# Kernel tuning notes

Hardware: AMD Instinct MI355X
Metric: run time of the kernel (lower is better)

## Reference

```python
import jax, jax.numpy as jnp
import numpy as np

TAU = 0.25
VTH = 1.0

def setup_inputs() -> dict:
    key = jax.random.key(0)
    k1, k2 = jax.random.split(key)
    B, T, F, U = 256, 100, 1024, 1024
    x = jax.random.normal(k1, (B, T, F), dtype=jnp.float32)
    kernel = jax.random.normal(k2, (F, U), dtype=jnp.float32) * 0.02
    bias = jnp.zeros((U,), dtype=jnp.float32)
    return {"x": x, "kernel": kernel, "bias": bias}

def reference(x, kernel, bias):
    # x: [B, T, F]; one big GEMM for all timesteps, then sequential LIF scan.
    current = jnp.einsum('btf,fu->btu', x, kernel) + bias  # [B, T, U]
    B, T, U = current.shape
    v0 = jnp.zeros((B, U), dtype=x.dtype)

    def lif_step(voltage, cur_t):
        voltage = TAU * voltage + (1.0 - TAU) * cur_t
        spikes = (voltage > VTH).astype(cur_t.dtype)
        voltage = voltage - spikes * VTH
        return voltage, spikes

    _, spikes_t = jax.lax.scan(lif_step, v0, jnp.moveaxis(current, 1, 0))  # [T, B, U]
    output_spikes = jnp.moveaxis(spikes_t, 0, 1)  # [B, T, U]
    spike_counts = jnp.sum(output_spikes, axis=1)  # [B, U]
    return output_spikes, spike_counts
```

## Files before the change

### kernel.cpp

```cpp
#include <hip/hip_runtime.h>


#define UN 128
#define BK 16
#define CS 132
#define CHUNK 50
#define TMAX 100

__device__ __forceinline__ void gload_lds16(const float* g, float* l) {
    __builtin_amdgcn_global_load_lds(
        (const __attribute__((address_space(1))) void*)g,
        (__attribute__((address_space(3))) void*)l,
        16, 0, 0);
}

__global__ __launch_bounds__(256) void fused_snn(
    const float* __restrict__ x,
    const float* __restrict__ W,
    const float* __restrict__ bias,
    float* __restrict__ spikes,
    float* __restrict__ counts,
    int B, int T, int F, int U)
{
    __shared__ __align__(16) float smem[CHUNK * CS];
    float* As = smem;
    float* Ws = smem + 1600;

    const int tid = threadIdx.x;
    const int tg  = tid >> 4;
    const int ug  = tid & 15;
    const int u0  = blockIdx.x * UN;
    const int b   = blockIdx.y;

    float acc[7][8];
    #pragma unroll
    for (int i = 0; i < 7; i++)
        #pragma unroll
        for (int j = 0; j < 8; j++) acc[i][j] = 0.f;

    const float* xb = x + (size_t)b * T * F;

    const float* ga0 = xb + (size_t)(tid >> 2) * F + (tid & 3) * 4;
    const float* ga1 = xb + (size_t)(64 + (tid >> 2)) * F + (tid & 3) * 4;
    const float* gw0 = W + (size_t)(tid >> 5) * U + u0 + (tid & 31) * 4;
    const float* gw1 = W + (size_t)(8 + (tid >> 5)) * U + u0 + (tid & 31) * 4;
    float* la0 = As + tid * 4;
    float* la1 = As + (256 + tid) * 4;
    float* lw0 = Ws + tid * 4;
    float* lw1 = Ws + (256 + tid) * 4;
    const bool a1on = (tid < 144);
    const bool w0   = (tid < 64);

    for (int k0 = 0; k0 < F; k0 += BK) {
        gload_lds16(ga0 + k0, la0);
        if (a1on) gload_lds16(ga1 + k0, la1);
        gload_lds16(gw0 + (size_t)k0 * U, lw0);
        gload_lds16(gw1 + (size_t)k0 * U, lw1);
        __syncthreads();

        const float* ap = As + tg * 16;
        const float* wp = Ws + ug * 4;
        #pragma unroll 1
        for (int kk = 0; kk < BK; kk += 2) {
            float4 b0 = *(const float4*)(wp + kk * 128);
            float4 b1 = *(const float4*)(wp + kk * 128 + 64);
            float4 b2 = *(const float4*)(wp + kk * 128 + 128);
            float4 b3 = *(const float4*)(wp + kk * 128 + 192);
            #pragma unroll
            for (int i = 0; i < 6; i++) {
                float2 a = *(const float2*)(ap + i * 256 + kk);
                acc[i][0] += a.x * b0.x;  acc[i][1] += a.x * b0.y;
                acc[i][2] += a.x * b0.z;  acc[i][3] += a.x * b0.w;
                acc[i][4] += a.x * b1.x;  acc[i][5] += a.x * b1.y;
                acc[i][6] += a.x * b1.z;  acc[i][7] += a.x * b1.w;
                acc[i][0] += a.y * b2.x;  acc[i][1] += a.y * b2.y;
                acc[i][2] += a.y * b2.z;  acc[i][3] += a.y * b2.w;
                acc[i][4] += a.y * b3.x;  acc[i][5] += a.y * b3.y;
                acc[i][6] += a.y * b3.z;  acc[i][7] += a.y * b3.w;
            }
            if (w0) {
                float2 a = *(const float2*)(ap + 6 * 256 + kk);
                acc[6][0] += a.x * b0.x;  acc[6][1] += a.x * b0.y;
                acc[6][2] += a.x * b0.z;  acc[6][3] += a.x * b0.w;
                acc[6][4] += a.x * b1.x;  acc[6][5] += a.x * b1.y;
                acc[6][6] += a.x * b1.z;  acc[6][7] += a.x * b1.w;
                acc[6][0] += a.y * b2.x;  acc[6][1] += a.y * b2.y;
                acc[6][2] += a.y * b2.z;  acc[6][3] += a.y * b2.w;
                acc[6][4] += a.y * b3.x;  acc[6][5] += a.y * b3.y;
                acc[6][6] += a.y * b3.z;  acc[6][7] += a.y * b3.w;
            }
        }
        __syncthreads();
    }

    float bb[8];
    {
        float4 bv0 = *(const float4*)(bias + u0 + 4 * ug);
        float4 bv1 = *(const float4*)(bias + u0 + 64 + 4 * ug);
        bb[0] = bv0.x; bb[1] = bv0.y; bb[2] = bv0.z; bb[3] = bv0.w;
        bb[4] = bv1.x; bb[5] = bv1.y; bb[6] = bv1.z; bb[7] = bv1.w;
    }

    float v = 0.f, cnt = 0.f;
    float* sp = spikes + (size_t)b * T * U + u0 + tid;

    #pragma unroll
    for (int c = 0; c < 2; c++) {
        #pragma unroll
        for (int i = 0; i < 7; i++) {
            const int t = i * 16 + tg;
            if (t >= c * CHUNK && t < c * CHUNK + CHUNK && t < TMAX) {
                const int r = t - c * CHUNK;
                float4 c0, c1;
                c0.x = acc[i][0] + bb[0]; c0.y = acc[i][1] + bb[1];
                c0.z = acc[i][2] + bb[2]; c0.w = acc[i][3] + bb[3];
                c1.x = acc[i][4] + bb[4]; c1.y = acc[i][5] + bb[5];
                c1.z = acc[i][6] + bb[6]; c1.w = acc[i][7] + bb[7];
                *(float4*)(smem + r * CS + 4 * ug)      = c0;
                *(float4*)(smem + r * CS + 64 + 4 * ug) = c1;
            }
        }
        __syncthreads();
        if (tid < UN) {
#pragma clang fp contract(off)
            for (int r = 0; r < CHUNK; r++) {
                float cval = smem[r * CS + tid];
                v = 0.25f * v + 0.75f * cval;
                float s = (v > 1.0f) ? 1.0f : 0.0f;
                v -= s;
                cnt += s;
                sp[(size_t)(c * CHUNK + r) * U] = s;
            }
        }
        __syncthreads();
    }
    if (tid < UN) counts[(size_t)b * U + u0 + tid] = cnt;
}

extern "C" void kernel_launch(void* const* d_in, const int* in_sizes, int n_in,
                              void* d_out, int out_size, void* d_ws, size_t ws_size,
                              hipStream_t stream) {
    const float* x    = (const float*)d_in[0];
    const float* kern = (const float*)d_in[1];
    const float* bias = (const float*)d_in[2];
    float* out = (float*)d_out;

    const int U = in_sizes[2];
    const int F = in_sizes[1] / U;
    const int R = in_sizes[0] / F;
    const int B = out_size / U - R;
    const int T = R / B;

    float* spikes = out;
    float* counts = out + (size_t)R * U;

    dim3 grid(U / UN, B);
    fused_snn<<<grid, 256, 0, stream>>>(x, kern, bias, spikes, counts,
                                        B, T, F, U);
}
```

Measured before the change: 735.9 us.

## Double-buffer x tiles in LDS and read weights directly from global

```diff
diff --git a/kernel.cpp b/kernel.cpp
--- a/kernel.cpp
+++ b/kernel.cpp
@@ -23,8 +23,8 @@
     int B, int T, int F, int U)
 {
     __shared__ __align__(16) float smem[CHUNK * CS];
-    float* As = smem;
-    float* Ws = smem + 1600;
+    float* As0 = smem;
+    float* As1 = smem + 1600;
 
     const int tid = threadIdx.x;
     const int tg  = tid >> 4;
@@ -42,56 +42,68 @@
 
     const float* ga0 = xb + (size_t)(tid >> 2) * F + (tid & 3) * 4;
     const float* ga1 = xb + (size_t)(64 + (tid >> 2)) * F + (tid & 3) * 4;
-    const float* gw0 = W + (size_t)(tid >> 5) * U + u0 + (tid & 31) * 4;
-    const float* gw1 = W + (size_t)(8 + (tid >> 5)) * U + u0 + (tid & 31) * 4;
-    float* la0 = As + tid * 4;
-    float* la1 = As + (256 + tid) * 4;
-    float* lw0 = Ws + tid * 4;
-    float* lw1 = Ws + (256 + tid) * 4;
+    const int la0 = tid * 4;
+    const int la1 = (256 + tid) * 4;
     const bool a1on = (tid < 144);
     const bool w0   = (tid < 64);
 
-    for (int k0 = 0; k0 < F; k0 += BK) {
-        gload_lds16(ga0 + k0, la0);
-        if (a1on) gload_lds16(ga1 + k0, la1);
-        gload_lds16(gw0 + (size_t)k0 * U, lw0);
-        gload_lds16(gw1 + (size_t)k0 * U, lw1);
+#define STAGE(buf, kof)                                   \
+    do {                                                  \
+        gload_lds16(ga0 + (kof), (buf) + la0);            \
+        if (a1on) gload_lds16(ga1 + (kof), (buf) + la1);  \
+    } while (0)
+
+#define COMPUTE(buf, k0b)                                                  \
+    do {                                                                   \
+        const float* ap = (buf) + tg * 16;                                 \
+        _Pragma("unroll 1")                                                \
+        for (int kk = 0; kk < BK; kk += 2) {                               \
+            const float* wk = W + (size_t)((k0b) + kk) * U + u0;           \
+            float4 b0 = *(const float4*)(wk + 4 * ug);                     \
+            float4 b1 = *(const float4*)(wk + 64 + 4 * ug);                \
+            float4 b2 = *(const float4*)(wk + U + 4 * ug);                 \
+            float4 b3 = *(const float4*)(wk + U + 64 + 4 * ug);            \
+            _Pragma("unroll")                                              \
+            for (int i = 0; i < 6; i++) {                                  \
+                float2 a = *(const float2*)(ap + i * 256 + kk);            \
+                acc[i][0] += a.x * b0.x;  acc[i][1] += a.x * b0.y;         \
+                acc[i][2] += a.x * b0.z;  acc[i][3] += a.x * b0.w;         \
+                acc[i][4] += a.x * b1.x;  acc[i][5] += a.x * b1.y;         \
+                acc[i][6] += a.x * b1.z;  acc[i][7] += a.x * b1.w;         \
+                acc[i][0] += a.y * b2.x;  acc[i][1] += a.y * b2.y;         \
+                acc[i][2] += a.y * b2.z;  acc[i][3] += a.y * b2.w;         \
+                acc[i][4] += a.y * b3.x;  acc[i][5] += a.y * b3.y;         \
+                acc[i][6] += a.y * b3.z;  acc[i][7] += a.y * b3.w;         \
+            }                                                              \
+            if (w0) {     \
+                float2 a = *(const float2*)(ap + 6 * 256 + kk);            \
+                acc[6][0] += a.x * b0.x;  acc[6][1] += a.x * b0.y;         \
+                acc[6][2] += a.x * b0.z;  acc[6][3] += a.x * b0.w;         \
+                acc[6][4] += a.x * b1.x;  acc[6][5] += a.x * b1.y;         \
+                acc[6][6] += a.x * b1.z;  acc[6][7] += a.x * b1.w;         \
+                acc[6][0] += a.y * b2.x;  acc[6][1] += a.y * b2.y;         \
+                acc[6][2] += a.y * b2.z;  acc[6][3] += a.y * b2.w;         \
+                acc[6][4] += a.y * b3.x;  acc[6][5] += a.y * b3.y;         \
+                acc[6][6] += a.y * b3.z;  acc[6][7] += a.y * b3.w;         \
+            }                                                              \
+        }                                                                  \
+    } while (0)
+
+    STAGE(As0, 0);
+    __syncthreads();
+
+    #pragma unroll 1
+    for (int k0 = 0; k0 < F; k0 += 2 * BK) {
+        STAGE(As1, k0 + BK);
+        COMPUTE(As0, k0);
         __syncthreads();
-
-        const float* ap = As + tg * 16;
-        const float* wp = Ws + ug * 4;
-        #pragma unroll 1
-        for (int kk = 0; kk < BK; kk += 2) {
-            float4 b0 = *(const float4*)(wp + kk * 128);
-            float4 b1 = *(const float4*)(wp + kk * 128 + 64);
-            float4 b2 = *(const float4*)(wp + kk * 128 + 128);
-            float4 b3 = *(const float4*)(wp + kk * 128 + 192);
-            #pragma unroll
-            for (int i = 0; i < 6; i++) {
-                float2 a = *(const float2*)(ap + i * 256 + kk);
-                acc[i][0] += a.x * b0.x;  acc[i][1] += a.x * b0.y;
-                acc[i][2] += a.x * b0.z;  acc[i][3] += a.x * b0.w;
-                acc[i][4] += a.x * b1.x;  acc[i][5] += a.x * b1.y;
-                acc[i][6] += a.x * b1.z;  acc[i][7] += a.x * b1.w;
-                acc[i][0] += a.y * b2.x;  acc[i][1] += a.y * b2.y;
-                acc[i][2] += a.y * b2.z;  acc[i][3] += a.y * b2.w;
-                acc[i][4] += a.y * b3.x;  acc[i][5] += a.y * b3.y;
-                acc[i][6] += a.y * b3.z;  acc[i][7] += a.y * b3.w;
-            }
-            if (w0) {
-                float2 a = *(const float2*)(ap + 6 * 256 + kk);
-                acc[6][0] += a.x * b0.x;  acc[6][1] += a.x * b0.y;
-                acc[6][2] += a.x * b0.z;  acc[6][3] += a.x * b0.w;
-                acc[6][4] += a.x * b1.x;  acc[6][5] += a.x * b1.y;
-                acc[6][6] += a.x * b1.z;  acc[6][7] += a.x * b1.w;
-                acc[6][0] += a.y * b2.x;  acc[6][1] += a.y * b2.y;
-                acc[6][2] += a.y * b2.z;  acc[6][3] += a.y * b2.w;
-                acc[6][4] += a.y * b3.x;  acc[6][5] += a.y * b3.y;
-                acc[6][6] += a.y * b3.z;  acc[6][7] += a.y * b3.w;
-            }
-        }
+        if (k0 + 2 * BK < F) STAGE(As0, k0 + 2 * BK);
+        COMPUTE(As1, k0 + BK);
         __syncthreads();
     }
+
+#undef STAGE
+#undef COMPUTE
 
     float bb[8];
     {
```

New measurement: 850.6 us. +15.6%, slower.
